# Kernel optimization log

Hardware: AMD Instinct MI355X
Metric: run time of the kernel (lower is better)

Reference implementation:

```python
import jax, jax.numpy as jnp
import numpy as np

KNOTS = 16
BOUND = 5.0
BATCH = 500000
X_DIM = 6          # split into lower(3) / upper(3)
C_DIM = 4
HID = 128
SPLINE_DIM = 3 * KNOTS - 1   # 47 (non-periodic)
LOWER = X_DIM // 2
OUT_DIM = LOWER * SPLINE_DIM


def setup_inputs() -> dict:
    key = jax.random.key(0)
    ks = jax.random.split(key, 10)
    def glorot(k, shape):
        fan_in, fan_out = shape
        s = jnp.sqrt(2.0 / (fan_in + fan_out))
        return (jax.random.normal(k, shape, jnp.float32) * s)
    return {
        "x": jax.random.normal(ks[0], (BATCH, X_DIM), jnp.float32),
        "c": jax.random.normal(ks[1], (BATCH, C_DIM), jnp.float32),
        "W1": glorot(ks[2], (LOWER + C_DIM + 0 + (X_DIM - LOWER), HID))[: X_DIM - LOWER + C_DIM],
        "b1": jnp.zeros((HID,), jnp.float32),
        "W2": glorot(ks[3], (HID, HID)),
        "b2": jnp.zeros((HID,), jnp.float32),
        "W3": glorot(ks[4], (HID, OUT_DIM)),
        "b3": jnp.zeros((OUT_DIM,), jnp.float32),
        "train": False,
    }


def _mlp(h, W1, b1, W2, b2, W3, b3):
    h = jax.nn.relu(h @ W1 + b1)
    h = jax.nn.relu(h @ W2 + b2)
    return h @ W3 + b3


def _rqs_forward(x, W, H, D, B):
    """Rational-quadratic spline (Durkan et al.) forward.
    x: [N,d]; W,H: [N,d,K] bin widths/heights; D: [N,d,K-1] interior derivs."""
    K = W.shape[-1]
    pad = jnp.full(W.shape[:-1] + (1,), -B, W.dtype)
    xk = jnp.concatenate([pad, -B + jnp.cumsum(W, axis=-1)], axis=-1)  # [N,d,K+1]
    yk = jnp.concatenate([pad, -B + jnp.cumsum(H, axis=-1)], axis=-1)
    one = jnp.ones(D.shape[:-1] + (1,), D.dtype)
    dk = jnp.concatenate([one, D, one], axis=-1)                        # [N,d,K+1]

    oob = (x <= -B) | (x >= B)
    xm = jnp.where(oob, -B, x)
    # bin index per element (searchsorted via comparison-sum)
    idx = jnp.clip(jnp.sum((xm[..., None] >= xk), axis=-1) - 1, 0, K - 1)[..., None]

    gat = lambda a, i: jnp.take_along_axis(a, i, axis=-1)[..., 0]
    xk_b = gat(xk, idx)
    yk_b = gat(yk, idx)
    wk = gat(xk, idx + 1) - xk_b
    hk = gat(yk, idx + 1) - yk_b
    dk_b = gat(dk, idx)
    dk1 = gat(dk, idx + 1)

    sk = hk / wk
    relx = jnp.clip((xm - xk_b) / wk, 0.0, 1.0)
    r1 = relx * (1.0 - relx)
    den = sk + (dk1 + dk_b - 2.0 * sk) * r1
    num = hk * (sk * relx * relx + dk_b * r1)
    y = yk_b + num / den
    ld = (2.0 * jnp.log(sk)
          + jnp.log(dk1 * relx * relx + 2.0 * sk * r1 + dk_b * (1.0 - relx) ** 2)
          - 2.0 * jnp.log(den))

    y = jnp.where(oob, x, y)
    ld = jnp.where(oob, 0.0, ld)
    return y, jnp.sum(ld, axis=1)


def reference(x, c, W1, b1, W2, b2, W3, b3, train):
    lower, upper = x[:, :LOWER], x[:, LOWER:]
    h = jnp.hstack((upper, c))
    p = _mlp(h, W1, b1, W2, b2, W3, b3)
    p = p.reshape(-1, LOWER, SPLINE_DIM)
    Wb, Hb, Db = jnp.split(p, [KNOTS, 2 * KNOTS], axis=2)
    Wb = 2.0 * BOUND * jax.nn.softmax(Wb, axis=-1)
    Hb = 2.0 * BOUND * jax.nn.softmax(Hb, axis=-1)
    Db = jax.nn.softplus(Db)
    lo_t, log_det = _rqs_forward(lower, Wb, Hb, Db, BOUND)
    y = jnp.hstack((lo_t, upper))
    return y, log_det
```

## Files before the change

### kernel.cpp

```cpp
#include <hip/hip_runtime.h>
#include <math.h>


#define TILE 128
#define NT   512
#define HID  128
#define OUTD 141
#define SRS  152
#define BND  5.0f
#define T1   0.5413248546f

typedef __bf16 bf16;
typedef _Float16 f16;
typedef __attribute__((ext_vector_type(8))) __bf16 bf16x8;
typedef __attribute__((ext_vector_type(8))) _Float16 f16x8;
typedef __attribute__((ext_vector_type(4))) _Float16 f16x4;
typedef __attribute__((ext_vector_type(2))) _Float16 f16x2;
typedef __attribute__((ext_vector_type(4))) float f32x4;

#define W3BASE 0
#define W1BASE 2304
#define W2BASE 2816
#define NFRAG  4864
#define B3P_OFF (NFRAG * 16)

#define SMEM_BYTES 79360

__global__ void nsc_prepack(const float* __restrict__ W1, const float* __restrict__ W2,
                            const float* __restrict__ W3, const float* __restrict__ b3,
                            bf16* __restrict__ Wall, float* __restrict__ b3p) {
    int f = blockIdx.x * 256 + threadIdx.x;
    int lane = f & 63, lm = lane & 15, lq = lane >> 4;
    if (f < W1BASE) {
        int tk = f >> 6, t3 = tk >> 2, kc = tk & 3;
        int col = t3 * 16 + lm;
        bf16x8 pk;
        #pragma unroll
        for (int j = 0; j < 8; ++j) {
            int feat = ((kc * 2 + (j >> 2)) << 4) + (lq << 2) + (j & 3);
            pk[j] = (col < OUTD) ? (bf16)W3[feat * OUTD + col] : (bf16)0.f;
        }
        *(bf16x8*)&Wall[(size_t)f * 8] = pk;
    } else if (f < W2BASE) {
        int t = (f - W1BASE) >> 6;
        int m = t * 16 + lm;
        bf16x8 pk;
        #pragma unroll
        for (int j = 0; j < 8; ++j) {
            int k = lq * 8 + j;
            pk[j] = (k < 7) ? (bf16)W1[k * HID + m] : (bf16)0.f;
        }
        *(bf16x8*)&Wall[(size_t)f * 8] = pk;
    } else if (f < NFRAG) {
        int tk = (f - W2BASE) >> 6, t2 = tk >> 2, kc = tk & 3;
        int m = t2 * 16 + lm;
        bf16x8 pk;
        #pragma unroll
        for (int j = 0; j < 8; ++j) {
            int feat = ((kc * 2 + (j >> 2)) << 4) + (lq << 2) + (j & 3);
            pk[j] = (bf16)W2[feat * HID + m];
        }
        *(bf16x8*)&Wall[(size_t)f * 8] = pk;
    } else if (f < NFRAG + 144) {
        int i = f - NFRAG;
        b3p[i] = (i < OUTD) ? b3[i] : 0.f;
    }
}

__global__ __launch_bounds__(NT, 4) void nsc_main(
    const float* __restrict__ x, const float* __restrict__ c,
    const bf16* __restrict__ Wall, const float* __restrict__ b1,
    const float* __restrict__ b2, const float* __restrict__ b3p,
    float* __restrict__ out_y, float* __restrict__ out_ld, int N)
{
    __shared__ __align__(16) char smem[SMEM_BYTES];
    bf16*  wlds  = (bf16*)smem;
    f16*   shp16 = (f16*)(smem + 36864);
    float* shld  = (float*)(smem + 77824);

    const int tid  = threadIdx.x;
    const int g0   = blockIdx.x * TILE;
    const int lane = tid & 63;
    const int wv   = tid >> 6;
    const int lm   = lane & 15;
    const int lq   = lane >> 4;
    const int sbase = wv * 16;

    float vin[8];
    #pragma unroll
    for (int j = 0; j < 8; ++j) vin[j] = 0.f;
    {
        int g = g0 + sbase + lm;
        if (lq == 0 && g < N) {
            vin[0] = x[g * 6 + 3]; vin[1] = x[g * 6 + 4];
            vin[2] = x[g * 6 + 5];
            vin[3] = c[g * 4];     vin[4] = c[g * 4 + 1];
            vin[5] = c[g * 4 + 2]; vin[6] = c[g * 4 + 3];
        }
    }

    {
        const float4* src = (const float4*)Wall;
        float4* dst = (float4*)smem;
        #pragma unroll
        for (int j = 0; j < 10; ++j) {
            int idx = tid + j * NT;
            if (idx < NFRAG) dst[idx] = src[idx];
        }
    }
    __syncthreads();

    bf16x8 inb;
    {
        bf16x8 t;
        #pragma unroll
        for (int j = 0; j < 8; ++j) t[j] = (bf16)vin[j];
        inb = t;
    }

    f32x4 acc1[8];
    {
        #pragma unroll
        for (int t = 0; t < 8; ++t)
            acc1[t] = *(const f32x4*)&b1[t * 16 + lq * 4];
        #pragma unroll
        for (int t = 0; t < 8; ++t) {
            bf16x8 wf = *(const bf16x8*)&wlds[(size_t)((W1BASE + t * 64 + lane)) * 8];
            acc1[t] = __builtin_amdgcn_mfma_f32_16x16x32_bf16(wf, inb, acc1[t], 0, 0, 0);
        }
    }
    bf16x8 h1B[4];
    #pragma unroll
    for (int kc = 0; kc < 4; ++kc) {
        bf16x8 hb;
        #pragma unroll
        for (int j = 0; j < 8; ++j)
            hb[j] = (bf16)fmaxf(acc1[kc * 2 + (j >> 2)][j & 3], 0.f);
        h1B[kc] = hb;
    }

    bf16x8 h2B[4];
    #pragma unroll
    for (int tp = 0; tp < 4; ++tp) {
        f32x4 acc[2];
        #pragma unroll
        for (int dt = 0; dt < 2; ++dt)
            acc[dt] = *(const f32x4*)&b2[(tp * 2 + dt) * 16 + lq * 4];
        #pragma unroll
        for (int kc = 0; kc < 4; ++kc)
            #pragma unroll
            for (int dt = 0; dt < 2; ++dt) {
                bf16x8 wf = *(const bf16x8*)&wlds[(size_t)((W2BASE + ((tp * 2 + dt) * 4 + kc) * 64 + lane)) * 8];
                acc[dt] = __builtin_amdgcn_mfma_f32_16x16x32_bf16(wf, h1B[kc], acc[dt], 0, 0, 0);
            }
        bf16x8 hb;
        #pragma unroll
        for (int j = 0; j < 8; ++j)
            hb[j] = (bf16)fmaxf(acc[j >> 2][j & 3], 0.f);
        h2B[tp] = hb;
    }
    __syncthreads();

    #pragma unroll
    for (int t3 = 0; t3 < 9; ++t3) {
        f32x4 acc = *(const f32x4*)&b3p[t3 * 16 + lq * 4];
        #pragma unroll
        for (int kc = 0; kc < 4; ++kc) {
            bf16x8 wf = *(const bf16x8*)&wlds[(size_t)((W3BASE + (t3 * 4 + kc) * 64 + lane)) * 8];
            acc = __builtin_amdgcn_mfma_f32_16x16x32_bf16(wf, h2B[kc], acc, 0, 0, 0);
        }
        {
            int s = sbase + lm;
            f16x4 pk = (f16x4){(f16)acc[0], (f16)acc[1],
                               (f16)acc[2], (f16)acc[3]};
            int off = t3 * 16 + lq * 4;
            if (t3 < 8) {
                *(f16x4*)&shp16[s * SRS + off] = pk;
            } else {
                if (lq < 3) *(f16x4*)&shp16[s * SRS + off] = pk;
                else        shp16[s * SRS + 140] = pk[0];
            }
        }
    }
    __syncthreads();

    if (wv < 6) {
        const int grp = wv;
        const int d = grp >> 1;
        const int s = ((grp & 1) << 6) + lane;
        const int g = g0 + s;
        if (g < N) {
            const f16* pr = &shp16[s * SRS];
            float w_[16], h_[16], dl[15];
            if (d == 0) {
                f16x8 A0 = *(const f16x8*)&pr[0],  A1 = *(const f16x8*)&pr[8];
                f16x8 A2 = *(const f16x8*)&pr[16], A3 = *(const f16x8*)&pr[24];
                f16x8 A4 = *(const f16x8*)&pr[32], A5 = *(const f16x8*)&pr[40];
                #pragma unroll
                for (int i = 0; i < 8; ++i) {
                    w_[i] = (float)A0[i]; w_[8 + i] = (float)A1[i];
                    h_[i] = (float)A2[i]; h_[8 + i] = (float)A3[i];
                    dl[i] = (float)A4[i];
                }
                #pragma unroll
                for (int i = 0; i < 7; ++i) dl[8 + i] = (float)A5[i];
            } else if (d == 1) {
                float a47 = (float)pr[47];
                f16x8 A0 = *(const f16x8*)&pr[48], A1 = *(const f16x8*)&pr[56];
                f16x8 A2 = *(const f16x8*)&pr[64], A3 = *(const f16x8*)&pr[72];
                f16x8 A4 = *(const f16x8*)&pr[80], A5 = *(const f16x8*)&pr[88];
                w_[0] = a47;
                #pragma unroll
                for (int i = 0; i < 8; ++i) w_[1 + i] = (float)A0[i];
                #pragma unroll
                for (int i = 0; i < 7; ++i) w_[9 + i] = (float)A1[i];
                h_[0] = (float)A1[7];
                #pragma unroll
                for (int i = 0; i < 8; ++i) h_[1 + i] = (float)A2[i];
                #pragma unroll
                for (int i = 0; i < 7; ++i) h_[9 + i] = (float)A3[i];
                dl[0] = (float)A3[7];
                #pragma unroll
                for (int i = 0; i < 8; ++i) dl[1 + i] = (float)A4[i];
                #pragma unroll
                for (int i = 0; i < 6; ++i) dl[9 + i] = (float)A5[i];
            } else {
                f16x2 B  = *(const f16x2*)&pr[94];
                f16x8 C0 = *(const f16x8*)&pr[96],  C1 = *(const f16x8*)&pr[104];
                f16x8 C2 = *(const f16x8*)&pr[112], C3 = *(const f16x8*)&pr[120];
                f16x8 C4 = *(const f16x8*)&pr[128], E  = *(const f16x8*)&pr[136];
                w_[0] = (float)B[0]; w_[1] = (float)B[1];
                #pragma unroll
                for (int i = 0; i < 8; ++i) w_[2 + i] = (float)C0[i];
                #pragma unroll
                for (int i = 0; i < 6; ++i) w_[10 + i] = (float)C1[i];
                h_[0] = (float)C1[6]; h_[1] = (float)C1[7];
                #pragma unroll
                for (int i = 0; i < 8; ++i) h_[2 + i] = (float)C2[i];
                #pragma unroll
                for (int i = 0; i < 6; ++i) h_[10 + i] = (float)C3[i];
                dl[0] = (float)C3[6]; dl[1] = (float)C3[7];
                #pragma unroll
                for (int i = 0; i < 8; ++i) dl[2 + i] = (float)C4[i];
                #pragma unroll
                for (int i = 0; i < 5; ++i) dl[10 + i] = (float)E[i];
            }

            float sw = 0.f, sh = 0.f;
            #pragma unroll
            for (int i = 0; i < 16; ++i) { w_[i] = __expf(w_[i]); sw += w_[i]; }
            #pragma unroll
            for (int i = 0; i < 16; ++i) { h_[i] = __expf(h_[i]); sh += h_[i]; }
            float cwn = 10.f * __builtin_amdgcn_rcpf(sw);
            float chn = 10.f * __builtin_amdgcn_rcpf(sh);
            #pragma unroll
            for (int i = 0; i < 16; ++i) { w_[i] *= cwn; h_[i] *= chn; }

            float xv = x[g * 6 + d];
            bool oob = (xv <= -BND) || (xv >= BND);
            float xm = oob ? -BND : xv;

            float cumx = -BND + w_[0], cumy = -BND + h_[0];
            float xk_b = -BND, yk_b = -BND;
            float wk = w_[0], hk = h_[0];
            float d0l = T1, d1l = dl[0];
            #pragma unroll
            for (int i = 1; i < 16; ++i) {
                bool ge = (xm >= cumx);
                if (ge) {
                    xk_b = cumx; yk_b = cumy;
                    wk = w_[i]; hk = h_[i];
                    d0l = dl[i - 1];
                    d1l = (i < 15) ? dl[i] : T1;
                }
                cumx += w_[i]; cumy += h_[i];
            }
            float d0 = (d0l > 15.f) ? d0l : __logf(1.f + __expf(d0l));
            float d1 = (d1l > 15.f) ? d1l : __logf(1.f + __expf(d1l));

            float rwk = __builtin_amdgcn_rcpf(wk);
            float sk = hk * rwk;
            float relx = (xm - xk_b) * rwk;
            relx = fminf(fmaxf(relx, 0.f), 1.f);
            float r1 = relx * (1.f - relx);
            float den = sk + (d1 + d0 - 2.f * sk) * r1;
            float iden = __builtin_amdgcn_rcpf(den);
            float num = hk * (sk * relx * relx + d0 * r1);
            float y = yk_b + num * iden;
            float omr = 1.f - relx;
            float arg = d1 * relx * relx + 2.f * sk * r1 + d0 * omr * omr;
            float ratio = sk * iden;
            float ld = __logf(ratio * ratio * arg);
            if (oob) { y = xv; ld = 0.f; }

            out_y[g * 6 + d] = y;
            out_y[g * 6 + 3 + d] = x[g * 6 + 3 + d];
            shld[s * 3 + d] = ld;
        }
    }
    __syncthreads();

    if (tid < TILE) {
        int g = g0 + tid;
        if (g < N)
            out_ld[g] = shld[tid * 3] + shld[tid * 3 + 1] + shld[tid * 3 + 2];
    }
}

extern "C" void kernel_launch(void* const* d_in, const int* in_sizes, int n_in,
                              void* d_out, int out_size, void* d_ws, size_t ws_size,
                              hipStream_t stream) {
    const float* x  = (const float*)d_in[0];
    const float* c  = (const float*)d_in[1];
    const float* W1 = (const float*)d_in[2];
    const float* b1 = (const float*)d_in[3];
    const float* W2 = (const float*)d_in[4];
    const float* b2 = (const float*)d_in[5];
    const float* W3 = (const float*)d_in[6];
    const float* b3 = (const float*)d_in[7];

    const int N = in_sizes[0] / 6;
    float* out_y  = (float*)d_out;
    float* out_ld = (float*)d_out + (size_t)N * 6;

    bf16*  Wall = (bf16*)d_ws;
    float* b3p  = (float*)((char*)d_ws + B3P_OFF);

    int nthreads = NFRAG + 144;
    nsc_prepack<<<(nthreads + 255) / 256, 256, 0, stream>>>(W1, W2, W3, b3,
                                                            Wall, b3p);

    int nblocks = (N + TILE - 1) / TILE;
    nsc_main<<<nblocks, NT, 0, stream>>>(x, c, Wall, b1, b2, b3p,
                                         out_y, out_ld, N);
}
```

Before: 146.3 us.

## Make MLP-spline kernel persistent with 32x32 MFMA and input prefetch

Launches a fixed grid of 256 persistent blocks that stage the packed bf16 weights into LDS once and then loop over 256-row tiles. Before, every 128-row tile reloaded about 78 KB of weights. The weight prepacking and all three MLP layers move from 16x16x32 to 32x32x16 bf16 MFMA fragments. The next tile's x/c inputs are prefetched into registers while the current tile computes. In exchange, LDS use grows to about 155 KB per block, which limits each CU to one 8-wave block and lowers latency hiding, and the spline stage now runs in two rounds per wave.

```diff
diff --git a/kernel.cpp b/kernel.cpp
--- a/kernel.cpp
+++ b/kernel.cpp
@@ -2,8 +2,9 @@
 #include <math.h>
 
 
-#define TILE 128
+#define TILE 256
 #define NT   512
+#define NBLK 256
 #define HID  128
 #define OUTD 141
 #define SRS  152
@@ -17,57 +18,60 @@
 typedef __attribute__((ext_vector_type(4))) _Float16 f16x4;
 typedef __attribute__((ext_vector_type(2))) _Float16 f16x2;
 typedef __attribute__((ext_vector_type(4))) float f32x4;
+typedef __attribute__((ext_vector_type(16))) float f32x16;
 
 #define W3BASE 0
-#define W1BASE 2304
+#define W1BASE 2560
 #define W2BASE 2816
 #define NFRAG  4864
 #define B3P_OFF (NFRAG * 16)
 
-#define SMEM_BYTES 79360
+#define SHP_OFF   77824
+#define SHLD_OFF  155648
+#define SMEM_BYTES 158720
 
 __global__ void nsc_prepack(const float* __restrict__ W1, const float* __restrict__ W2,
                             const float* __restrict__ W3, const float* __restrict__ b3,
                             bf16* __restrict__ Wall, float* __restrict__ b3p) {
     int f = blockIdx.x * 256 + threadIdx.x;
-    int lane = f & 63, lm = lane & 15, lq = lane >> 4;
+    int lane = f & 63, ln = lane & 31, h = lane >> 5;
     if (f < W1BASE) {
-        int tk = f >> 6, t3 = tk >> 2, kc = tk & 3;
-        int col = t3 * 16 + lm;
+        int u = f >> 6, t3 = u >> 3, kc = u & 7;
+        int col = t3 * 32 + ln;
         bf16x8 pk;
         #pragma unroll
         for (int j = 0; j < 8; ++j) {
-            int feat = ((kc * 2 + (j >> 2)) << 4) + (lq << 2) + (j & 3);
+            int feat = kc * 16 + (j & 3) + 8 * (j >> 2) + 4 * h;
             pk[j] = (col < OUTD) ? (bf16)W3[feat * OUTD + col] : (bf16)0.f;
         }
         *(bf16x8*)&Wall[(size_t)f * 8] = pk;
     } else if (f < W2BASE) {
         int t = (f - W1BASE) >> 6;
-        int m = t * 16 + lm;
+        int m = t * 32 + ln;
         bf16x8 pk;
         #pragma unroll
         for (int j = 0; j < 8; ++j) {
-            int k = lq * 8 + j;
-            pk[j] = (k < 7) ? (bf16)W1[k * HID + m] : (bf16)0.f;
+            int feat = (j & 3) + 8 * (j >> 2) + 4 * h;
+            pk[j] = (feat < 7) ? (bf16)W1[feat * HID + m] : (bf16)0.f;
         }
         *(bf16x8*)&Wall[(size_t)f * 8] = pk;
     } else if (f < NFRAG) {
-        int tk = (f - W2BASE) >> 6, t2 = tk >> 2, kc = tk & 3;
-        int m = t2 * 16 + lm;
+        int u = (f - W2BASE) >> 6, t2 = u >> 3, kc = u & 7;
+        int m = t2 * 32 + ln;
         bf16x8 pk;
         #pragma unroll
         for (int j = 0; j < 8; ++j) {
-            int feat = ((kc * 2 + (j >> 2)) << 4) + (lq << 2) + (j & 3);
+            int feat = kc * 16 + (j & 3) + 8 * (j >> 2) + 4 * h;
             pk[j] = (bf16)W2[feat * HID + m];
         }
         *(bf16x8*)&Wall[(size_t)f * 8] = pk;
-    } else if (f < NFRAG + 144) {
+    } else if (f < NFRAG + 160) {
         int i = f - NFRAG;
         b3p[i] = (i < OUTD) ? b3[i] : 0.f;
     }
 }
 
-__global__ __launch_bounds__(NT, 4) void nsc_main(
+__global__ __launch_bounds__(NT, 2) void nsc_main(
     const float* __restrict__ x, const float* __restrict__ c,
     const bf16* __restrict__ Wall, const float* __restrict__ b1,
     const float* __restrict__ b2, const float* __restrict__ b3p,
@@ -75,27 +79,27 @@
 {
     __shared__ __align__(16) char smem[SMEM_BYTES];
     bf16*  wlds  = (bf16*)smem;
-    f16*   shp16 = (f16*)(smem + 36864);
-    float* shld  = (float*)(smem + 77824);
+    f16*   shp16 = (f16*)(smem + SHP_OFF);
+    float* shld  = (float*)(smem + SHLD_OFF);
 
     const int tid  = threadIdx.x;
-    const int g0   = blockIdx.x * TILE;
     const int lane = tid & 63;
     const int wv   = tid >> 6;
-    const int lm   = lane & 15;
-    const int lq   = lane >> 4;
-    const int sbase = wv * 16;
-
-    float vin[8];
-    #pragma unroll
-    for (int j = 0; j < 8; ++j) vin[j] = 0.f;
-    {
-        int g = g0 + sbase + lm;
-        if (lq == 0 && g < N) {
-            vin[0] = x[g * 6 + 3]; vin[1] = x[g * 6 + 4];
-            vin[2] = x[g * 6 + 5];
-            vin[3] = c[g * 4];     vin[4] = c[g * 4 + 1];
-            vin[5] = c[g * 4 + 2]; vin[6] = c[g * 4 + 3];
+    const int ln   = lane & 31;
+    const int h    = lane >> 5;
+    const int sbase = wv * 32;
+    const int ntiles = (N + TILE - 1) / TILE;
+
+    int T = blockIdx.x;
+
+    float vcur[4] = {0.f, 0.f, 0.f, 0.f};
+    if (T < ntiles) {
+        int g = T * TILE + sbase + ln;
+        if (g < N) {
+            if (h == 0) { vcur[0] = x[g*6+3]; vcur[1] = x[g*6+4];
+                          vcur[2] = x[g*6+5]; vcur[3] = c[g*4]; }
+            else        { vcur[0] = c[g*4+1]; vcur[1] = c[g*4+2];
+                          vcur[2] = c[g*4+3]; }
         }
     }
 
@@ -110,200 +114,248 @@
     }
     __syncthreads();
 
-    bf16x8 inb;
-    {
-        bf16x8 t;
-        #pragma unroll
-        for (int j = 0; j < 8; ++j) t[j] = (bf16)vin[j];
-        inb = t;
-    }
-
-    f32x4 acc1[8];
-    {
-        #pragma unroll
-        for (int t = 0; t < 8; ++t)
-            acc1[t] = *(const f32x4*)&b1[t * 16 + lq * 4];
-        #pragma unroll
-        for (int t = 0; t < 8; ++t) {
-            bf16x8 wf = *(const bf16x8*)&wlds[(size_t)((W1BASE + t * 64 + lane)) * 8];
-            acc1[t] = __builtin_amdgcn_mfma_f32_16x16x32_bf16(wf, inb, acc1[t], 0, 0, 0);
-        }
-    }
-    bf16x8 h1B[4];
-    #pragma unroll
-    for (int kc = 0; kc < 4; ++kc) {
-        bf16x8 hb;
-        #pragma unroll
-        for (int j = 0; j < 8; ++j)
-            hb[j] = (bf16)fmaxf(acc1[kc * 2 + (j >> 2)][j & 3], 0.f);
-        h1B[kc] = hb;
-    }
-
-    bf16x8 h2B[4];
-    #pragma unroll
-    for (int tp = 0; tp < 4; ++tp) {
-        f32x4 acc[2];
-        #pragma unroll
-        for (int dt = 0; dt < 2; ++dt)
-            acc[dt] = *(const f32x4*)&b2[(tp * 2 + dt) * 16 + lq * 4];
-        #pragma unroll
-        for (int kc = 0; kc < 4; ++kc)
-            #pragma unroll
-            for (int dt = 0; dt < 2; ++dt) {
-                bf16x8 wf = *(const bf16x8*)&wlds[(size_t)((W2BASE + ((tp * 2 + dt) * 4 + kc) * 64 + lane)) * 8];
-                acc[dt] = __builtin_amdgcn_mfma_f32_16x16x32_bf16(wf, h1B[kc], acc[dt], 0, 0, 0);
-            }
-        bf16x8 hb;
-        #pragma unroll
-        for (int j = 0; j < 8; ++j)
-            hb[j] = (bf16)fmaxf(acc[j >> 2][j & 3], 0.f);
-        h2B[tp] = hb;
-    }
-    __syncthreads();
-
-    #pragma unroll
-    for (int t3 = 0; t3 < 9; ++t3) {
-        f32x4 acc = *(const f32x4*)&b3p[t3 * 16 + lq * 4];
-        #pragma unroll
-        for (int kc = 0; kc < 4; ++kc) {
-            bf16x8 wf = *(const bf16x8*)&wlds[(size_t)((W3BASE + (t3 * 4 + kc) * 64 + lane)) * 8];
-            acc = __builtin_amdgcn_mfma_f32_16x16x32_bf16(wf, h2B[kc], acc, 0, 0, 0);
-        }
+    for (; T < ntiles; T += NBLK) {
+        bf16x8 inb;
+        inb[0] = (bf16)vcur[0]; inb[1] = (bf16)vcur[1];
+        inb[2] = (bf16)vcur[2]; inb[3] = (bf16)vcur[3];
+        inb[4] = (bf16)0.f; inb[5] = (bf16)0.f; inb[6] = (bf16)0.f; inb[7] = (bf16)0.f;
+
+        float vnext[4] = {0.f, 0.f, 0.f, 0.f};
         {
-            int s = sbase + lm;
-            f16x4 pk = (f16x4){(f16)acc[0], (f16)acc[1],
-                               (f16)acc[2], (f16)acc[3]};
-            int off = t3 * 16 + lq * 4;
-            if (t3 < 8) {
-                *(f16x4*)&shp16[s * SRS + off] = pk;
-            } else {
-                if (lq < 3) *(f16x4*)&shp16[s * SRS + off] = pk;
-                else        shp16[s * SRS + 140] = pk[0];
-            }
-        }
-    }
-    __syncthreads();
-
-    if (wv < 6) {
-        const int grp = wv;
-        const int d = grp >> 1;
-        const int s = ((grp & 1) << 6) + lane;
-        const int g = g0 + s;
-        if (g < N) {
-            const f16* pr = &shp16[s * SRS];
-            float w_[16], h_[16], dl[15];
-            if (d == 0) {
-                f16x8 A0 = *(const f16x8*)&pr[0],  A1 = *(const f16x8*)&pr[8];
-                f16x8 A2 = *(const f16x8*)&pr[16], A3 = *(const f16x8*)&pr[24];
-                f16x8 A4 = *(const f16x8*)&pr[32], A5 = *(const f16x8*)&pr[40];
-                #pragma unroll
-                for (int i = 0; i < 8; ++i) {
-                    w_[i] = (float)A0[i]; w_[8 + i] = (float)A1[i];
-                    h_[i] = (float)A2[i]; h_[8 + i] = (float)A3[i];
-                    dl[i] = (float)A4[i];
-                }
-                #pragma unroll
-                for (int i = 0; i < 7; ++i) dl[8 + i] = (float)A5[i];
-            } else if (d == 1) {
-                float a47 = (float)pr[47];
-                f16x8 A0 = *(const f16x8*)&pr[48], A1 = *(const f16x8*)&pr[56];
-                f16x8 A2 = *(const f16x8*)&pr[64], A3 = *(const f16x8*)&pr[72];
-                f16x8 A4 = *(const f16x8*)&pr[80], A5 = *(const f16x8*)&pr[88];
-                w_[0] = a47;
-                #pragma unroll
-                for (int i = 0; i < 8; ++i) w_[1 + i] = (float)A0[i];
-                #pragma unroll
-                for (int i = 0; i < 7; ++i) w_[9 + i] = (float)A1[i];
-                h_[0] = (float)A1[7];
-                #pragma unroll
-                for (int i = 0; i < 8; ++i) h_[1 + i] = (float)A2[i];
-                #pragma unroll
-                for (int i = 0; i < 7; ++i) h_[9 + i] = (float)A3[i];
-                dl[0] = (float)A3[7];
-                #pragma unroll
-                for (int i = 0; i < 8; ++i) dl[1 + i] = (float)A4[i];
-                #pragma unroll
-                for (int i = 0; i < 6; ++i) dl[9 + i] = (float)A5[i];
-            } else {
-                f16x2 B  = *(const f16x2*)&pr[94];
-                f16x8 C0 = *(const f16x8*)&pr[96],  C1 = *(const f16x8*)&pr[104];
-                f16x8 C2 = *(const f16x8*)&pr[112], C3 = *(const f16x8*)&pr[120];
-                f16x8 C4 = *(const f16x8*)&pr[128], E  = *(const f16x8*)&pr[136];
-                w_[0] = (float)B[0]; w_[1] = (float)B[1];
-                #pragma unroll
-                for (int i = 0; i < 8; ++i) w_[2 + i] = (float)C0[i];
-                #pragma unroll
-                for (int i = 0; i < 6; ++i) w_[10 + i] = (float)C1[i];
-                h_[0] = (float)C1[6]; h_[1] = (float)C1[7];
-                #pragma unroll
-                for (int i = 0; i < 8; ++i) h_[2 + i] = (float)C2[i];
-                #pragma unroll
-                for (int i = 0; i < 6; ++i) h_[10 + i] = (float)C3[i];
-                dl[0] = (float)C3[6]; dl[1] = (float)C3[7];
-                #pragma unroll
-                for (int i = 0; i < 8; ++i) dl[2 + i] = (float)C4[i];
-                #pragma unroll
-                for (int i = 0; i < 5; ++i) dl[10 + i] = (float)E[i];
-            }
-
-            float sw = 0.f, sh = 0.f;
-            #pragma unroll
-            for (int i = 0; i < 16; ++i) { w_[i] = __expf(w_[i]); sw += w_[i]; }
-            #pragma unroll
-            for (int i = 0; i < 16; ++i) { h_[i] = __expf(h_[i]); sh += h_[i]; }
-            float cwn = 10.f * __builtin_amdgcn_rcpf(sw);
-            float chn = 10.f * __builtin_amdgcn_rcpf(sh);
-            #pragma unroll
-            for (int i = 0; i < 16; ++i) { w_[i] *= cwn; h_[i] *= chn; }
-
-            float xv = x[g * 6 + d];
-            bool oob = (xv <= -BND) || (xv >= BND);
-            float xm = oob ? -BND : xv;
-
-            float cumx = -BND + w_[0], cumy = -BND + h_[0];
-            float xk_b = -BND, yk_b = -BND;
-            float wk = w_[0], hk = h_[0];
-            float d0l = T1, d1l = dl[0];
-            #pragma unroll
-            for (int i = 1; i < 16; ++i) {
-                bool ge = (xm >= cumx);
-                if (ge) {
-                    xk_b = cumx; yk_b = cumy;
-                    wk = w_[i]; hk = h_[i];
-                    d0l = dl[i - 1];
-                    d1l = (i < 15) ? dl[i] : T1;
-                }
-                cumx += w_[i]; cumy += h_[i];
-            }
-            float d0 = (d0l > 15.f) ? d0l : __logf(1.f + __expf(d0l));
-            float d1 = (d1l > 15.f) ? d1l : __logf(1.f + __expf(d1l));
-
-            float rwk = __builtin_amdgcn_rcpf(wk);
-            float sk = hk * rwk;
-            float relx = (xm - xk_b) * rwk;
-            relx = fminf(fmaxf(relx, 0.f), 1.f);
-            float r1 = relx * (1.f - relx);
-            float den = sk + (d1 + d0 - 2.f * sk) * r1;
-            float iden = __builtin_amdgcn_rcpf(den);
-            float num = hk * (sk * relx * relx + d0 * r1);
-            float y = yk_b + num * iden;
-            float omr = 1.f - relx;
-            float arg = d1 * relx * relx + 2.f * sk * r1 + d0 * omr * omr;
-            float ratio = sk * iden;
-            float ld = __logf(ratio * ratio * arg);
-            if (oob) { y = xv; ld = 0.f; }
-
-            out_y[g * 6 + d] = y;
-            out_y[g * 6 + 3 + d] = x[g * 6 + 3 + d];
-            shld[s * 3 + d] = ld;
-        }
-    }
-    __syncthreads();
-
-    if (tid < TILE) {
-        int g = g0 + tid;
-        if (g < N)
-            out_ld[g] = shld[tid * 3] + shld[tid * 3 + 1] + shld[tid * 3 + 2];
+            int Tn = T + NBLK;
+            if (Tn < ntiles) {
+                int g = Tn * TILE + sbase + ln;
+                if (g < N) {
+                    if (h == 0) { vnext[0] = x[g*6+3]; vnext[1] = x[g*6+4];
+                                  vnext[2] = x[g*6+5]; vnext[3] = c[g*4]; }
+                    else        { vnext[0] = c[g*4+1]; vnext[1] = c[g*4+2];
+                                  vnext[2] = c[g*4+3]; }
+                }
+            }
+        }
+
+        f32x16 acc1[4];
+        #pragma unroll
+        for (int t = 0; t < 4; ++t) {
+            #pragma unroll
+            for (int q = 0; q < 4; ++q) {
+                f32x4 bb = *(const f32x4*)&b1[t*32 + 4*h + 8*q];
+                acc1[t][4*q+0] = bb[0]; acc1[t][4*q+1] = bb[1];
+                acc1[t][4*q+2] = bb[2]; acc1[t][4*q+3] = bb[3];
+            }
+        }
+        #pragma unroll
+        for (int t = 0; t < 4; ++t) {
+            bf16x8 wf = *(const bf16x8*)&wlds[(size_t)(W1BASE + t*64 + lane) * 8];
+            acc1[t] = __builtin_amdgcn_mfma_f32_32x32x16_bf16(wf, inb, acc1[t], 0, 0, 0);
+        }
+        bf16x8 B2[8];
+        #pragma unroll
+        for (int t = 0; t < 4; ++t)
+            #pragma unroll
+            for (int cc = 0; cc < 2; ++cc) {
+                bf16x8 hb;
+                #pragma unroll
+                for (int j = 0; j < 8; ++j)
+                    hb[j] = (bf16)fmaxf(acc1[t][8*cc + j], 0.f);
+                B2[2*t + cc] = hb;
+            }
+
+        f32x16 acc2[4];
+        #pragma unroll
+        for (int t2 = 0; t2 < 4; ++t2) {
+            #pragma unroll
+            for (int q = 0; q < 4; ++q) {
+                f32x4 bb = *(const f32x4*)&b2[t2*32 + 4*h + 8*q];
+                acc2[t2][4*q+0] = bb[0]; acc2[t2][4*q+1] = bb[1];
+                acc2[t2][4*q+2] = bb[2]; acc2[t2][4*q+3] = bb[3];
+            }
+        }
+        #pragma unroll
+        for (int t2 = 0; t2 < 4; ++t2)
+            #pragma unroll
+            for (int kc = 0; kc < 8; ++kc) {
+                bf16x8 wf = *(const bf16x8*)&wlds[(size_t)(W2BASE + (t2*8 + kc)*64 + lane) * 8];
+                acc2[t2] = __builtin_amdgcn_mfma_f32_32x32x16_bf16(wf, B2[kc], acc2[t2], 0, 0, 0);
+            }
+        bf16x8 B3f[8];
+        #pragma unroll
+        for (int t2 = 0; t2 < 4; ++t2)
+            #pragma unroll
+            for (int cc = 0; cc < 2; ++cc) {
+                bf16x8 hb;
+                #pragma unroll
+                for (int j = 0; j < 8; ++j)
+                    hb[j] = (bf16)fmaxf(acc2[t2][8*cc + j], 0.f);
+                B3f[2*t2 + cc] = hb;
+            }
+        __syncthreads();
+
+        {
+            const int s = sbase + ln;
+            #pragma unroll
+            for (int t3 = 0; t3 < 5; ++t3) {
+                f32x16 a3;
+                #pragma unroll
+                for (int q = 0; q < 4; ++q) {
+                    f32x4 bb = *(const f32x4*)&b3p[t3*32 + 4*h + 8*q];
+                    a3[4*q+0] = bb[0]; a3[4*q+1] = bb[1];
+                    a3[4*q+2] = bb[2]; a3[4*q+3] = bb[3];
+                }
+                #pragma unroll
+                for (int kc = 0; kc < 8; ++kc) {
+                    bf16x8 wf = *(const bf16x8*)&wlds[(size_t)(W3BASE + (t3*8 + kc)*64 + lane) * 8];
+                    a3 = __builtin_amdgcn_mfma_f32_32x32x16_bf16(wf, B3f[kc], a3, 0, 0, 0);
+                }
+                if (t3 < 4) {
+                    #pragma unroll
+                    for (int q = 0; q < 4; ++q) {
+                        f16x4 pk = (f16x4){(f16)a3[4*q+0], (f16)a3[4*q+1],
+                                           (f16)a3[4*q+2], (f16)a3[4*q+3]};
+                        *(f16x4*)&shp16[s*SRS + t3*32 + 4*h + 8*q] = pk;
+                    }
+                } else {
+                    if (h == 0) {
+                        f16x4 p0 = (f16x4){(f16)a3[0], (f16)a3[1], (f16)a3[2], (f16)a3[3]};
+                        f16x4 p1 = (f16x4){(f16)a3[4], (f16)a3[5], (f16)a3[6], (f16)a3[7]};
+                        *(f16x4*)&shp16[s*SRS + 128] = p0;
+                        *(f16x4*)&shp16[s*SRS + 136] = p1;
+                    } else {
+                        f16x4 p0 = (f16x4){(f16)a3[0], (f16)a3[1], (f16)a3[2], (f16)a3[3]};
+                        *(f16x4*)&shp16[s*SRS + 132] = p0;
+                        shp16[s*SRS + 140] = (f16)a3[4];
+                    }
+                }
+            }
+        }
+        __syncthreads();
+
+        #pragma unroll 1
+        for (int rr = 0; rr < 2; ++rr) {
+            if (rr == 1 && wv < 4) break;
+            const int grp = (rr == 0) ? wv : (wv + 4);
+            const int d = grp >> 2;
+            const int s = (grp & 3) * 64 + lane;
+            const int g = T * TILE + s;
+            if (g < N) {
+                const f16* pr = &shp16[s * SRS];
+                float w_[16], h_[16], dl[15];
+                if (d == 0) {
+                    f16x8 A0 = *(const f16x8*)&pr[0],  A1 = *(const f16x8*)&pr[8];
+                    f16x8 A2 = *(const f16x8*)&pr[16], A3 = *(const f16x8*)&pr[24];
+                    f16x8 A4 = *(const f16x8*)&pr[32], A5 = *(const f16x8*)&pr[40];
+                    #pragma unroll
+                    for (int i = 0; i < 8; ++i) {
+                        w_[i] = (float)A0[i]; w_[8 + i] = (float)A1[i];
+                        h_[i] = (float)A2[i]; h_[8 + i] = (float)A3[i];
+                        dl[i] = (float)A4[i];
+                    }
+                    #pragma unroll
+                    for (int i = 0; i < 7; ++i) dl[8 + i] = (float)A5[i];
+                } else if (d == 1) {
+                    float a47 = (float)pr[47];
+                    f16x8 A0 = *(const f16x8*)&pr[48], A1 = *(const f16x8*)&pr[56];
+                    f16x8 A2 = *(const f16x8*)&pr[64], A3 = *(const f16x8*)&pr[72];
+                    f16x8 A4 = *(const f16x8*)&pr[80], A5 = *(const f16x8*)&pr[88];
+                    w_[0] = a47;
+                    #pragma unroll
+                    for (int i = 0; i < 8; ++i) w_[1 + i] = (float)A0[i];
+                    #pragma unroll
+                    for (int i = 0; i < 7; ++i) w_[9 + i] = (float)A1[i];
+                    h_[0] = (float)A1[7];
+                    #pragma unroll
+                    for (int i = 0; i < 8; ++i) h_[1 + i] = (float)A2[i];
+                    #pragma unroll
+                    for (int i = 0; i < 7; ++i) h_[9 + i] = (float)A3[i];
+                    dl[0] = (float)A3[7];
+                    #pragma unroll
+                    for (int i = 0; i < 8; ++i) dl[1 + i] = (float)A4[i];
+                    #pragma unroll
+                    for (int i = 0; i < 6; ++i) dl[9 + i] = (float)A5[i];
+                } else {
+                    f16x2 B  = *(const f16x2*)&pr[94];
+                    f16x8 C0 = *(const f16x8*)&pr[96],  C1 = *(const f16x8*)&pr[104];
+                    f16x8 C2 = *(const f16x8*)&pr[112], C3 = *(const f16x8*)&pr[120];
+                    f16x8 C4 = *(const f16x8*)&pr[128], E  = *(const f16x8*)&pr[136];
+                    w_[0] = (float)B[0]; w_[1] = (float)B[1];
+                    #pragma unroll
+                    for (int i = 0; i < 8; ++i) w_[2 + i] = (float)C0[i];
+                    #pragma unroll
+                    for (int i = 0; i < 6; ++i) w_[10 + i] = (float)C1[i];
+                    h_[0] = (float)C1[6]; h_[1] = (float)C1[7];
+                    #pragma unroll
+                    for (int i = 0; i < 8; ++i) h_[2 + i] = (float)C2[i];
+                    #pragma unroll
+                    for (int i = 0; i < 6; ++i) h_[10 + i] = (float)C3[i];
+                    dl[0] = (float)C3[6]; dl[1] = (float)C3[7];
+                    #pragma unroll
+                    for (int i = 0; i < 8; ++i) dl[2 + i] = (float)C4[i];
+                    #pragma unroll
+                    for (int i = 0; i < 5; ++i) dl[10 + i] = (float)E[i];
+                }
+
+                float sw = 0.f, sh = 0.f;
+                #pragma unroll
+                for (int i = 0; i < 16; ++i) { w_[i] = __expf(w_[i]); sw += w_[i]; }
+                #pragma unroll
+                for (int i = 0; i < 16; ++i) { h_[i] = __expf(h_[i]); sh += h_[i]; }
+                float cwn = 10.f * __builtin_amdgcn_rcpf(sw);
+                float chn = 10.f * __builtin_amdgcn_rcpf(sh);
+                #pragma unroll
+                for (int i = 0; i < 16; ++i) { w_[i] *= cwn; h_[i] *= chn; }
+
+                float xv = x[g * 6 + d];
+                bool oob = (xv <= -BND) || (xv >= BND);
+                float xm = oob ? -BND : xv;
+
+                float cumx = -BND + w_[0], cumy = -BND + h_[0];
+                float xk_b = -BND, yk_b = -BND;
+                float wk = w_[0], hk = h_[0];
+                float d0l = T1, d1l = dl[0];
+                #pragma unroll
+                for (int i = 1; i < 16; ++i) {
+                    bool ge = (xm >= cumx);
+                    if (ge) {
+                        xk_b = cumx; yk_b = cumy;
+                        wk = w_[i]; hk = h_[i];
+                        d0l = dl[i - 1];
+                        d1l = (i < 15) ? dl[i] : T1;
+                    }
+                    cumx += w_[i]; cumy += h_[i];
+                }
+                float d0 = (d0l > 15.f) ? d0l : __logf(1.f + __expf(d0l));
+                float d1 = (d1l > 15.f) ? d1l : __logf(1.f + __expf(d1l));
+
+                float rwk = __builtin_amdgcn_rcpf(wk);
+                float sk = hk * rwk;
+                float relx = (xm - xk_b) * rwk;
+                relx = fminf(fmaxf(relx, 0.f), 1.f);
+                float r1 = relx * (1.f - relx);
+                float den = sk + (d1 + d0 - 2.f * sk) * r1;
+                float iden = __builtin_amdgcn_rcpf(den);
+                float num = hk * (sk * relx * relx + d0 * r1);
+                float y = yk_b + num * iden;
+                float omr = 1.f - relx;
+                float arg = d1 * relx * relx + 2.f * sk * r1 + d0 * omr * omr;
+                float ratio = sk * iden;
+                float ld = __logf(ratio * ratio * arg);
+                if (oob) { y = xv; ld = 0.f; }
+
+                out_y[g * 6 + d] = y;
+                out_y[g * 6 + 3 + d] = x[g * 6 + 3 + d];
+                shld[s * 3 + d] = ld;
+            }
+        }
+        __syncthreads();
+
+        if (tid < TILE) {
+            int g = T * TILE + tid;
+            if (g < N)
+                out_ld[g] = shld[tid * 3] + shld[tid * 3 + 1] + shld[tid * 3 + 2];
+        }
+
+        vcur[0] = vnext[0]; vcur[1] = vnext[1];
+        vcur[2] = vnext[2]; vcur[3] = vnext[3];
     }
 }
 
@@ -326,11 +378,10 @@
     bf16*  Wall = (bf16*)d_ws;
     float* b3p  = (float*)((char*)d_ws + B3P_OFF);
 
-    int nthreads = NFRAG + 144;
+    int nthreads = NFRAG + 160;
     nsc_prepack<<<(nthreads + 255) / 256, 256, 0, stream>>>(W1, W2, W3, b3,
                                                             Wall, b3p);
 
-    int nblocks = (N + TILE - 1) / TILE;
-    nsc_main<<<nblocks, NT, 0, stream>>>(x, c, Wall, b1, b2, b3p,
-                                         out_y, out_ld, N);
+    nsc_main<<<NBLK, NT, 0, stream>>>(x, c, Wall, b1, b2, b3p,
+                                      out_y, out_ld, N);
 }
```

Result: slower. 186.6 us (+27.5%).

## Process two 16-row sample sets per wave to double tile and reuse weight fragments

Applied to the files above, without the earlier changes.

The tile grows from 128 to 256 samples per block. Each wave now runs two 16-sample sets through the MLP, so every weight fragment loaded from LDS feeds two MFMAs. The spline parameter buffer is aliased over the weight region in LDS, and layer-3 results are held in registers until after a barrier, which keeps shared memory roughly the same size. The spline stage loops twice over waves to cover 256 samples. In exchange, register pressure rises under the (512,4) launch bounds, with a risk of spills or lower occupancy, and the grid has half as many blocks.

```diff
diff --git a/kernel.cpp b/kernel.cpp
--- a/kernel.cpp
+++ b/kernel.cpp
@@ -2,7 +2,7 @@
 #include <math.h>
 
 
-#define TILE 128
+#define TILE 256
 #define NT   512
 #define HID  128
 #define OUTD 141
@@ -24,7 +24,8 @@
 #define NFRAG  4864
 #define B3P_OFF (NFRAG * 16)
 
-#define SMEM_BYTES 79360
+#define SHLD_OFF  77824
+#define SMEM_BYTES 80896
 
 __global__ void nsc_prepack(const float* __restrict__ W1, const float* __restrict__ W2,
                             const float* __restrict__ W3, const float* __restrict__ b3,
@@ -75,8 +76,8 @@
 {
     __shared__ __align__(16) char smem[SMEM_BYTES];
     bf16*  wlds  = (bf16*)smem;
-    f16*   shp16 = (f16*)(smem + 36864);
-    float* shld  = (float*)(smem + 77824);
+    f16*   shp16 = (f16*)smem;
+    float* shld  = (float*)(smem + SHLD_OFF);
 
     const int tid  = threadIdx.x;
     const int g0   = blockIdx.x * TILE;
@@ -84,18 +85,19 @@
     const int wv   = tid >> 6;
     const int lm   = lane & 15;
     const int lq   = lane >> 4;
-    const int sbase = wv * 16;
-
-    float vin[8];
-    #pragma unroll
-    for (int j = 0; j < 8; ++j) vin[j] = 0.f;
-    {
-        int g = g0 + sbase + lm;
+    const int sbase = wv * 32;
+
+    float vin[2][8];
+    #pragma unroll
+    for (int set = 0; set < 2; ++set) {
+        #pragma unroll
+        for (int j = 0; j < 8; ++j) vin[set][j] = 0.f;
+        int g = g0 + sbase + set * 16 + lm;
         if (lq == 0 && g < N) {
-            vin[0] = x[g * 6 + 3]; vin[1] = x[g * 6 + 4];
-            vin[2] = x[g * 6 + 5];
-            vin[3] = c[g * 4];     vin[4] = c[g * 4 + 1];
-            vin[5] = c[g * 4 + 2]; vin[6] = c[g * 4 + 3];
+            vin[set][0] = x[g * 6 + 3]; vin[set][1] = x[g * 6 + 4];
+            vin[set][2] = x[g * 6 + 5];
+            vin[set][3] = c[g * 4];     vin[set][4] = c[g * 4 + 1];
+            vin[set][5] = c[g * 4 + 2]; vin[set][6] = c[g * 4 + 3];
         }
     }
 
@@ -110,84 +112,108 @@
     }
     __syncthreads();
 
-    bf16x8 inb;
-    {
+    bf16x8 inb[2];
+    #pragma unroll
+    for (int set = 0; set < 2; ++set) {
         bf16x8 t;
         #pragma unroll
-        for (int j = 0; j < 8; ++j) t[j] = (bf16)vin[j];
-        inb = t;
-    }
-
-    f32x4 acc1[8];
-    {
-        #pragma unroll
-        for (int t = 0; t < 8; ++t)
-            acc1[t] = *(const f32x4*)&b1[t * 16 + lq * 4];
-        #pragma unroll
-        for (int t = 0; t < 8; ++t) {
-            bf16x8 wf = *(const bf16x8*)&wlds[(size_t)((W1BASE + t * 64 + lane)) * 8];
-            acc1[t] = __builtin_amdgcn_mfma_f32_16x16x32_bf16(wf, inb, acc1[t], 0, 0, 0);
-        }
-    }
-    bf16x8 h1B[4];
+        for (int j = 0; j < 8; ++j) t[j] = (bf16)vin[set][j];
+        inb[set] = t;
+    }
+
+    bf16x8 h1B[2][4];
     #pragma unroll
     for (int kc = 0; kc < 4; ++kc) {
-        bf16x8 hb;
-        #pragma unroll
-        for (int j = 0; j < 8; ++j)
-            hb[j] = (bf16)fmaxf(acc1[kc * 2 + (j >> 2)][j & 3], 0.f);
-        h1B[kc] = hb;
-    }
-
-    bf16x8 h2B[4];
+        bf16x8 wf0 = *(const bf16x8*)&wlds[(size_t)((W1BASE + (2 * kc) * 64 + lane)) * 8];
+        bf16x8 wf1 = *(const bf16x8*)&wlds[(size_t)((W1BASE + (2 * kc + 1) * 64 + lane)) * 8];
+        f32x4 b0 = *(const f32x4*)&b1[(2 * kc) * 16 + lq * 4];
+        f32x4 b1v = *(const f32x4*)&b1[(2 * kc + 1) * 16 + lq * 4];
+        f32x4 a0s0 = __builtin_amdgcn_mfma_f32_16x16x32_bf16(wf0, inb[0], b0, 0, 0, 0);
+        f32x4 a0s1 = __builtin_amdgcn_mfma_f32_16x16x32_bf16(wf0, inb[1], b0, 0, 0, 0);
+        f32x4 a1s0 = __builtin_amdgcn_mfma_f32_16x16x32_bf16(wf1, inb[0], b1v, 0, 0, 0);
+        f32x4 a1s1 = __builtin_amdgcn_mfma_f32_16x16x32_bf16(wf1, inb[1], b1v, 0, 0, 0);
+        bf16x8 h0, h1;
+        #pragma unroll
+        for (int j = 0; j < 4; ++j) {
+            h0[j]     = (bf16)fmaxf(a0s0[j], 0.f);
+            h0[4 + j] = (bf16)fmaxf(a1s0[j], 0.f);
+            h1[j]     = (bf16)fmaxf(a0s1[j], 0.f);
+            h1[4 + j] = (bf16)fmaxf(a1s1[j], 0.f);
+        }
+        h1B[0][kc] = h0;
+        h1B[1][kc] = h1;
+    }
+
+    bf16x8 h2B[2][4];
     #pragma unroll
     for (int tp = 0; tp < 4; ++tp) {
-        f32x4 acc[2];
-        #pragma unroll
-        for (int dt = 0; dt < 2; ++dt)
-            acc[dt] = *(const f32x4*)&b2[(tp * 2 + dt) * 16 + lq * 4];
+        f32x4 acc[2][2];
+        #pragma unroll
+        for (int dt = 0; dt < 2; ++dt) {
+            f32x4 bb = *(const f32x4*)&b2[(tp * 2 + dt) * 16 + lq * 4];
+            acc[0][dt] = bb; acc[1][dt] = bb;
+        }
         #pragma unroll
         for (int kc = 0; kc < 4; ++kc)
             #pragma unroll
             for (int dt = 0; dt < 2; ++dt) {
                 bf16x8 wf = *(const bf16x8*)&wlds[(size_t)((W2BASE + ((tp * 2 + dt) * 4 + kc) * 64 + lane)) * 8];
-                acc[dt] = __builtin_amdgcn_mfma_f32_16x16x32_bf16(wf, h1B[kc], acc[dt], 0, 0, 0);
+                acc[0][dt] = __builtin_amdgcn_mfma_f32_16x16x32_bf16(wf, h1B[0][kc], acc[0][dt], 0, 0, 0);
+                acc[1][dt] = __builtin_amdgcn_mfma_f32_16x16x32_bf16(wf, h1B[1][kc], acc[1][dt], 0, 0, 0);
             }
-        bf16x8 hb;
-        #pragma unroll
-        for (int j = 0; j < 8; ++j)
-            hb[j] = (bf16)fmaxf(acc[j >> 2][j & 3], 0.f);
-        h2B[tp] = hb;
-    }
-    __syncthreads();
-
+        #pragma unroll
+        for (int set = 0; set < 2; ++set) {
+            bf16x8 hb;
+            #pragma unroll
+            for (int j = 0; j < 8; ++j)
+                hb[j] = (bf16)fmaxf(acc[set][j >> 2][j & 3], 0.f);
+            h2B[set][tp] = hb;
+        }
+    }
+
+    f16x4 pk[2][9];
     #pragma unroll
     for (int t3 = 0; t3 < 9; ++t3) {
-        f32x4 acc = *(const f32x4*)&b3p[t3 * 16 + lq * 4];
+        f32x4 acc[2];
+        {
+            f32x4 bb = *(const f32x4*)&b3p[t3 * 16 + lq * 4];
+            acc[0] = bb; acc[1] = bb;
+        }
         #pragma unroll
         for (int kc = 0; kc < 4; ++kc) {
             bf16x8 wf = *(const bf16x8*)&wlds[(size_t)((W3BASE + (t3 * 4 + kc) * 64 + lane)) * 8];
-            acc = __builtin_amdgcn_mfma_f32_16x16x32_bf16(wf, h2B[kc], acc, 0, 0, 0);
-        }
-        {
-            int s = sbase + lm;
-            f16x4 pk = (f16x4){(f16)acc[0], (f16)acc[1],
-                               (f16)acc[2], (f16)acc[3]};
+            acc[0] = __builtin_amdgcn_mfma_f32_16x16x32_bf16(wf, h2B[0][kc], acc[0], 0, 0, 0);
+            acc[1] = __builtin_amdgcn_mfma_f32_16x16x32_bf16(wf, h2B[1][kc], acc[1], 0, 0, 0);
+        }
+        #pragma unroll
+        for (int set = 0; set < 2; ++set)
+            pk[set][t3] = (f16x4){(f16)acc[set][0], (f16)acc[set][1],
+                                  (f16)acc[set][2], (f16)acc[set][3]};
+    }
+    __syncthreads();
+
+    #pragma unroll
+    for (int set = 0; set < 2; ++set) {
+        int s = sbase + set * 16 + lm;
+        #pragma unroll
+        for (int t3 = 0; t3 < 9; ++t3) {
             int off = t3 * 16 + lq * 4;
             if (t3 < 8) {
-                *(f16x4*)&shp16[s * SRS + off] = pk;
+                *(f16x4*)&shp16[s * SRS + off] = pk[set][t3];
             } else {
-                if (lq < 3) *(f16x4*)&shp16[s * SRS + off] = pk;
-                else        shp16[s * SRS + 140] = pk[0];
+                if (lq < 3) *(f16x4*)&shp16[s * SRS + off] = pk[set][t3];
+                else        shp16[s * SRS + 140] = pk[set][t3][0];
             }
         }
     }
     __syncthreads();
 
-    if (wv < 6) {
-        const int grp = wv;
-        const int d = grp >> 1;
-        const int s = ((grp & 1) << 6) + lane;
+    #pragma unroll 1
+    for (int rr = 0; rr < 2; ++rr) {
+        if (rr == 1 && wv >= 4) break;
+        const int grp = (rr == 0) ? wv : (8 + wv);
+        const int d = grp >> 2;
+        const int s = (grp & 3) * 64 + lane;
         const int g = g0 + s;
         if (g < N) {
             const f16* pr = &shp16[s * SRS];
@@ -226,9 +252,12 @@
                 for (int i = 0; i < 6; ++i) dl[9 + i] = (float)A5[i];
             } else {
                 f16x2 B  = *(const f16x2*)&pr[94];
-                f16x8 C0 = *(const f16x8*)&pr[96],  C1 = *(const f16x8*)&pr[104];
-                f16x8 C2 = *(const f16x8*)&pr[112], C3 = *(const f16x8*)&pr[120];
-                f16x8 C4 = *(const f16x8*)&pr[128], E  = *(const f16x8*)&pr[136];
+                f16x8 C0 = *(const f16x8*)&pr[96];
+                f16x8 C1 = *(const f16x8*)&pr[104];
+                f16x8 C2 = *(const f16x8*)&pr[112];
+                f16x8 C3 = *(const f16x8*)&pr[120];
+                f16x8 C4 = *(const f16x8*)&pr[128];
+                f16x8 E  = *(const f16x8*)&pr[136];
                 w_[0] = (float)B[0]; w_[1] = (float)B[1];
                 #pragma unroll
                 for (int i = 0; i < 8; ++i) w_[2 + i] = (float)C0[i];
```

Result: faster. 133.7 us (-8.6%).
